# Optimization experiments

Measured on AMD Instinct MI355X. Metric: run time of the kernel, lower is better.

Reference implementation:

```python
import jax, jax.numpy as jnp
import numpy as np

NUM_SEGMENTS = 2048
EPS = 1e-6

def setup_inputs() -> dict:
    key = jax.random.key(0)
    k1, k2 = jax.random.split(key)
    N, D = 1000000, 64
    x = jax.random.normal(k1, (N, D), dtype=jnp.float32)
    seg = jnp.sort(jax.random.randint(k2, (N,), 0, NUM_SEGMENTS, dtype=jnp.int32))
    return {"x": x, "seg": seg}

def reference(x, seg):
    # Per-segment SCALAR min/max over all nodes and features of each graph,
    # matching torch's x.min()/x.max() on each unbatched segment.
    row_min = jnp.min(x, axis=1)  # [N]
    row_max = jnp.max(x, axis=1)  # [N]
    g_min = jax.ops.segment_min(row_min, seg, num_segments=NUM_SEGMENTS)  # [G]
    g_max = jax.ops.segment_max(row_max, seg, num_segments=NUM_SEGMENTS)  # [G]
    mn = g_min[seg][:, None]  # [N,1]
    mx = g_max[seg][:, None]  # [N,1]
    return (x - mn) / (mx - mn + EPS)
```

## Files before the change

### kernel.cpp

```cpp
#include <hip/hip_runtime.h>

#define NSEG 2048
#define EPS 1e-6f
#define TROWS 256
#define TF4 (TROWS * 16)

typedef float nfloat4 __attribute__((ext_vector_type(4)));

__device__ __forceinline__ unsigned enc(float f) {
    unsigned u = __float_as_uint(f);
    return (u & 0x80000000u) ? ~u : (u | 0x80000000u);
}
__device__ __forceinline__ float dec(unsigned k) {
    unsigned u = (k & 0x80000000u) ? (k & 0x7FFFFFFFu) : ~k;
    return __uint_as_float(u);
}

__global__ void init_k(unsigned* __restrict__ mn_k, unsigned* __restrict__ mx_k) {
    int i = blockIdx.x * blockDim.x + threadIdx.x;
    if (i < NSEG) {
        mn_k[i] = 0xFFFFFFFFu;
        mx_k[i] = 0u;
    }
}

__device__ __forceinline__ void wave_reduce(float& mn, float& mx) {
#pragma unroll
    for (int off = 32; off; off >>= 1) {
        mn = fminf(mn, __shfl_xor(mn, off));
        mx = fmaxf(mx, __shfl_xor(mx, off));
    }
}

__global__ __launch_bounds__(256) void pass1(const float4* __restrict__ x4,
                                             const int* __restrict__ seg,
                                             unsigned* __restrict__ mn_k,
                                             unsigned* __restrict__ mx_k,
                                             int nrows) {
    const long n4 = (long)nrows * 16;
    const long base = (long)blockIdx.x * TF4;
    const int t = threadIdx.x;
    const int row0 = blockIdx.x * TROWS;
    const int rlast = min(row0 + TROWS, nrows) - 1;
    const int sf = seg[row0];
    const int sl = seg[rlast];

    if (sf == sl) {
        float lmin = INFINITY, lmax = -INFINITY;
#pragma unroll
        for (int i = 0; i < 16; ++i) {
            long f = base + (long)i * 256 + t;
            if (f < n4) {
                float4 v = x4[f];
                lmin = fminf(lmin, fminf(fminf(v.x, v.y), fminf(v.z, v.w)));
                lmax = fmaxf(lmax, fmaxf(fmaxf(v.x, v.y), fmaxf(v.z, v.w)));
            }
        }
        wave_reduce(lmin, lmax);
        if ((t & 63) == 0) {
            atomicMin(&mn_k[sf], enc(lmin));
            atomicMax(&mx_k[sf], enc(lmax));
        }
    } else {
        float amin = INFINITY, amax = -INFINITY;
        int as = -1;
#pragma unroll
        for (int i = 0; i < 16; ++i) {
            long f = base + (long)i * 256 + t;
            bool valid = f < n4;
            float lmin = INFINITY, lmax = -INFINITY;
            int s = -1;
            if (valid) {
                float4 v = x4[f];
                lmin = fminf(fminf(v.x, v.y), fminf(v.z, v.w));
                lmax = fmaxf(fmaxf(v.x, v.y), fmaxf(v.z, v.w));
                s = seg[(int)(f >> 4)];
            }
            int s0 = __shfl(s, 0);
            if (__all(s == s0 || !valid)) {
                if (s0 < 0) continue;
                wave_reduce(lmin, lmax);
                if ((t & 63) == 0) {
                    if (s0 != as) {
                        if (as >= 0) {
                            atomicMin(&mn_k[as], enc(amin));
                            atomicMax(&mx_k[as], enc(amax));
                        }
                        as = s0; amin = lmin; amax = lmax;
                    } else {
                        amin = fminf(amin, lmin);
                        amax = fmaxf(amax, lmax);
                    }
                }
            } else {
                if (valid) {
                    atomicMin(&mn_k[s], enc(lmin));
                    atomicMax(&mx_k[s], enc(lmax));
                }
            }
        }
        if ((t & 63) == 0 && as >= 0) {
            atomicMin(&mn_k[as], enc(amin));
            atomicMax(&mx_k[as], enc(amax));
        }
    }
}

__global__ void scalek(const unsigned* __restrict__ mn_k,
                       const unsigned* __restrict__ mx_k,
                       float2* __restrict__ prm) {
    int i = blockIdx.x * blockDim.x + threadIdx.x;
    if (i < NSEG) {
        float mn = dec(mn_k[i]);
        float mx = dec(mx_k[i]);
        float2 p;
        p.x = mn;
        p.y = 1.0f / (mx - mn + EPS);
        prm[i] = p;
    }
}

__global__ __launch_bounds__(256) void pass2(const float4* __restrict__ x4,
                                             const int* __restrict__ seg,
                                             const float2* __restrict__ prm,
                                             nfloat4* __restrict__ out4,
                                             long n4) {
    long g = (long)blockIdx.x * 256 + threadIdx.x;
    if (g >= n4) return;
    int row = (int)(g >> 4);
    int s = seg[row];
    float2 p = prm[s];
    float4 v = x4[g];
    nfloat4 o;
    o.x = (v.x - p.x) * p.y;
    o.y = (v.y - p.x) * p.y;
    o.z = (v.z - p.x) * p.y;
    o.w = (v.w - p.x) * p.y;
    __builtin_nontemporal_store(o, &out4[g]);
}

extern "C" void kernel_launch(void* const* d_in, const int* in_sizes, int n_in,
                              void* d_out, int out_size, void* d_ws, size_t ws_size,
                              hipStream_t stream) {
    const float* x = (const float*)d_in[0];
    const int* seg = (const int*)d_in[1];
    float* out = (float*)d_out;

    const int nrows = in_sizes[1];
    const long n4 = (long)out_size / 4;

    unsigned* mn_k = (unsigned*)d_ws;
    unsigned* mx_k = mn_k + NSEG;
    float2* prm = (float2*)(mx_k + NSEG);

    init_k<<<(NSEG + 255) / 256, 256, 0, stream>>>(mn_k, mx_k);

    int blocks1 = (nrows + TROWS - 1) / TROWS;
    pass1<<<blocks1, 256, 0, stream>>>((const float4*)x, seg, mn_k, mx_k, nrows);

    scalek<<<(NSEG + 255) / 256, 256, 0, stream>>>(mn_k, mx_k, prm);

    long blocks2 = (n4 + 255) / 256;
    pass2<<<(int)blocks2, 256, 0, stream>>>((const float4*)x, seg, prm,
                                            (nfloat4*)out, n4);
}
```

Measured before the change: 471.8 us.

## Fuse reduction and normalize passes into one cooperative persistent kernel

Merges the per-segment min/max pass, the scale computation and the normalize pass into one persistent cooperative kernel with a grid-wide sync. Each block recomputes the per-segment parameters into shared memory after the sync, and the second sweep revisits the same tiles the block reduced, which may let some re-reads of x hit in cache. This removes two kernel launches and the global parameter array. In exchange every block does a grid barrier and redundantly decodes all 2048 segment parameters, and the grid size is fixed at 1024 blocks.

```diff
diff --git a/kernel.cpp b/kernel.cpp
--- a/kernel.cpp
+++ b/kernel.cpp
@@ -1,9 +1,14 @@
 #include <hip/hip_runtime.h>
+#include <hip/hip_cooperative_groups.h>
+
+namespace cg = cooperative_groups;
 
 #define NSEG 2048
 #define EPS 1e-6f
 #define TROWS 256
 #define TF4 (TROWS * 16)
+#define GRID 1024
+#define BLK 256
 
 typedef float nfloat4 __attribute__((ext_vector_type(4)));
 
@@ -32,135 +37,134 @@
     }
 }
 
-__global__ __launch_bounds__(256) void pass1(const float4* __restrict__ x4,
-                                             const int* __restrict__ seg,
-                                             unsigned* __restrict__ mn_k,
-                                             unsigned* __restrict__ mx_k,
-                                             int nrows) {
+__global__ __launch_bounds__(BLK, 4) void fused(
+        const float4* __restrict__ x4,
+        const int* __restrict__ seg,
+        unsigned* __restrict__ mn_k,
+        unsigned* __restrict__ mx_k,
+        nfloat4* __restrict__ out4,
+        int nrows)
+{
+    __shared__ float2 sprm[NSEG];
     const long n4 = (long)nrows * 16;
-    const long base = (long)blockIdx.x * TF4;
+    const int nTiles = (nrows + TROWS - 1) / TROWS;
     const int t = threadIdx.x;
-    const int row0 = blockIdx.x * TROWS;
-    const int rlast = min(row0 + TROWS, nrows) - 1;
-    const int sf = seg[row0];
-    const int sl = seg[rlast];
 
-    if (sf == sl) {
-        float lmin = INFINITY, lmax = -INFINITY;
+    for (int tile = blockIdx.x; tile < nTiles; tile += gridDim.x) {
+        const long base = (long)tile * TF4;
+        const int row0 = tile * TROWS;
+        const int rlast = min(row0 + TROWS, nrows) - 1;
+        const int sf = seg[row0];
+        const int sl = seg[rlast];
+
+        if (sf == sl) {
+            float lmin = INFINITY, lmax = -INFINITY;
+#pragma unroll
+            for (int i = 0; i < 16; ++i) {
+                long f = base + (long)i * 256 + t;
+                if (f < n4) {
+                    float4 v = x4[f];
+                    lmin = fminf(lmin, fminf(fminf(v.x, v.y), fminf(v.z, v.w)));
+                    lmax = fmaxf(lmax, fmaxf(fmaxf(v.x, v.y), fmaxf(v.z, v.w)));
+                }
+            }
+            wave_reduce(lmin, lmax);
+            if ((t & 63) == 0) {
+                atomicMin(&mn_k[sf], enc(lmin));
+                atomicMax(&mx_k[sf], enc(lmax));
+            }
+        } else {
+            float amin = INFINITY, amax = -INFINITY;
+            int as = -1;
+#pragma unroll
+            for (int i = 0; i < 16; ++i) {
+                long f = base + (long)i * 256 + t;
+                bool valid = f < n4;
+                float lmin = INFINITY, lmax = -INFINITY;
+                int s = -1;
+                if (valid) {
+                    float4 v = x4[f];
+                    lmin = fminf(fminf(v.x, v.y), fminf(v.z, v.w));
+                    lmax = fmaxf(fmaxf(v.x, v.y), fmaxf(v.z, v.w));
+                    s = seg[(int)(f >> 4)];
+                }
+                int s0 = __shfl(s, 0);
+                if (__all(s == s0 || !valid)) {
+                    if (s0 < 0) continue;
+                    wave_reduce(lmin, lmax);
+                    if ((t & 63) == 0) {
+                        if (s0 != as) {
+                            if (as >= 0) {
+                                atomicMin(&mn_k[as], enc(amin));
+                                atomicMax(&mx_k[as], enc(amax));
+                            }
+                            as = s0; amin = lmin; amax = lmax;
+                        } else {
+                            amin = fminf(amin, lmin);
+                            amax = fmaxf(amax, lmax);
+                        }
+                    }
+                } else {
+                    if (valid) {
+                        atomicMin(&mn_k[s], enc(lmin));
+                        atomicMax(&mx_k[s], enc(lmax));
+                    }
+                }
+            }
+            if ((t & 63) == 0 && as >= 0) {
+                atomicMin(&mn_k[as], enc(amin));
+                atomicMax(&mx_k[as], enc(amax));
+            }
+        }
+    }
+
+    cg::this_grid().sync();
+
+#pragma unroll
+    for (int k = 0; k < NSEG / BLK; ++k) {
+        int s = k * BLK + t;
+        float mn = dec(mn_k[s]);
+        float mx = dec(mx_k[s]);
+        sprm[s] = make_float2(mn, 1.0f / (mx - mn + EPS));
+    }
+    __syncthreads();
+
+    for (int tile = blockIdx.x; tile < nTiles; tile += gridDim.x) {
+        const long base = (long)tile * TF4;
 #pragma unroll
         for (int i = 0; i < 16; ++i) {
             long f = base + (long)i * 256 + t;
             if (f < n4) {
+                int row = (int)(f >> 4);
+                int s = seg[row];
+                float2 p = sprm[s];
                 float4 v = x4[f];
-                lmin = fminf(lmin, fminf(fminf(v.x, v.y), fminf(v.z, v.w)));
-                lmax = fmaxf(lmax, fmaxf(fmaxf(v.x, v.y), fmaxf(v.z, v.w)));
+                nfloat4 o;
+                o.x = (v.x - p.x) * p.y;
+                o.y = (v.y - p.x) * p.y;
+                o.z = (v.z - p.x) * p.y;
+                o.w = (v.w - p.x) * p.y;
+                __builtin_nontemporal_store(o, &out4[f]);
             }
         }
-        wave_reduce(lmin, lmax);
-        if ((t & 63) == 0) {
-            atomicMin(&mn_k[sf], enc(lmin));
-            atomicMax(&mx_k[sf], enc(lmax));
-        }
-    } else {
-        float amin = INFINITY, amax = -INFINITY;
-        int as = -1;
-#pragma unroll
-        for (int i = 0; i < 16; ++i) {
-            long f = base + (long)i * 256 + t;
-            bool valid = f < n4;
-            float lmin = INFINITY, lmax = -INFINITY;
-            int s = -1;
-            if (valid) {
-                float4 v = x4[f];
-                lmin = fminf(fminf(v.x, v.y), fminf(v.z, v.w));
-                lmax = fmaxf(fmaxf(v.x, v.y), fmaxf(v.z, v.w));
-                s = seg[(int)(f >> 4)];
-            }
-            int s0 = __shfl(s, 0);
-            if (__all(s == s0 || !valid)) {
-                if (s0 < 0) continue;
-                wave_reduce(lmin, lmax);
-                if ((t & 63) == 0) {
-                    if (s0 != as) {
-                        if (as >= 0) {
-                            atomicMin(&mn_k[as], enc(amin));
-                            atomicMax(&mx_k[as], enc(amax));
-                        }
-                        as = s0; amin = lmin; amax = lmax;
-                    } else {
-                        amin = fminf(amin, lmin);
-                        amax = fmaxf(amax, lmax);
-                    }
-                }
-            } else {
-                if (valid) {
-                    atomicMin(&mn_k[s], enc(lmin));
-                    atomicMax(&mx_k[s], enc(lmax));
-                }
-            }
-        }
-        if ((t & 63) == 0 && as >= 0) {
-            atomicMin(&mn_k[as], enc(amin));
-            atomicMax(&mx_k[as], enc(amax));
-        }
     }
-}
-
-__global__ void scalek(const unsigned* __restrict__ mn_k,
-                       const unsigned* __restrict__ mx_k,
-                       float2* __restrict__ prm) {
-    int i = blockIdx.x * blockDim.x + threadIdx.x;
-    if (i < NSEG) {
-        float mn = dec(mn_k[i]);
-        float mx = dec(mx_k[i]);
-        float2 p;
-        p.x = mn;
-        p.y = 1.0f / (mx - mn + EPS);
-        prm[i] = p;
-    }
-}
-
-__global__ __launch_bounds__(256) void pass2(const float4* __restrict__ x4,
-                                             const int* __restrict__ seg,
-                                             const float2* __restrict__ prm,
-                                             nfloat4* __restrict__ out4,
-                                             long n4) {
-    long g = (long)blockIdx.x * 256 + threadIdx.x;
-    if (g >= n4) return;
-    int row = (int)(g >> 4);
-    int s = seg[row];
-    float2 p = prm[s];
-    float4 v = x4[g];
-    nfloat4 o;
-    o.x = (v.x - p.x) * p.y;
-    o.y = (v.y - p.x) * p.y;
-    o.z = (v.z - p.x) * p.y;
-    o.w = (v.w - p.x) * p.y;
-    __builtin_nontemporal_store(o, &out4[g]);
 }
 
 extern "C" void kernel_launch(void* const* d_in, const int* in_sizes, int n_in,
                               void* d_out, int out_size, void* d_ws, size_t ws_size,
                               hipStream_t stream) {
-    const float* x = (const float*)d_in[0];
+    const float4* x4 = (const float4*)d_in[0];
     const int* seg = (const int*)d_in[1];
-    float* out = (float*)d_out;
-
+    nfloat4* out4 = (nfloat4*)d_out;
     const int nrows = in_sizes[1];
-    const long n4 = (long)out_size / 4;
 
     unsigned* mn_k = (unsigned*)d_ws;
     unsigned* mx_k = mn_k + NSEG;
-    float2* prm = (float2*)(mx_k + NSEG);
 
     init_k<<<(NSEG + 255) / 256, 256, 0, stream>>>(mn_k, mx_k);
 
-    int blocks1 = (nrows + TROWS - 1) / TROWS;
-    pass1<<<blocks1, 256, 0, stream>>>((const float4*)x, seg, mn_k, mx_k, nrows);
-
-    scalek<<<(NSEG + 255) / 256, 256, 0, stream>>>(mn_k, mx_k, prm);
-
-    long blocks2 = (n4 + 255) / 256;
-    pass2<<<(int)blocks2, 256, 0, stream>>>((const float4*)x, seg, prm,
-                                            (nfloat4*)out, n4);
+    void* args[] = {(void*)&x4, (void*)&seg, (void*)&mn_k, (void*)&mx_k,
+                    (void*)&out4, (void*)&nrows};
+    hipLaunchCooperativeKernel((const void*)fused, dim3(GRID), dim3(BLK),
+                               args, 0, stream);
 }
```

Result: slower. 600.5 us (+27.3%).
